# Optimization experiments

Hardware: AMD Instinct MI355X
Metric: run time of the kernel (lower is better)

## Reference

```python
import jax, jax.numpy as jnp
import numpy as np

K = 3
EPS = 1e-16

def setup_inputs() -> dict:
    key = jax.random.key(0)
    k1, k2, k3 = jax.random.split(key, 3)
    x = jax.random.normal(k1, (4096, 256), dtype=jnp.float32)
    pos_l = jax.random.normal(k2, (4096, 3), dtype=jnp.float32)
    pos_h = jax.random.normal(k3, (16384, 3), dtype=jnp.float32)
    return {"x": x, "pos_l": pos_l, "pos_h": pos_h}

def reference(x, pos_l, pos_h):
    # Squared pairwise distances [N_h, N_l] via expansion (GEMM-friendly)
    d2 = (jnp.sum(pos_h * pos_h, axis=1)[:, None]
          - 2.0 * pos_h @ pos_l.T
          + jnp.sum(pos_l * pos_l, axis=1)[None, :])
    # k nearest coarse neighbors per fine point
    _, idx = jax.lax.top_k(-d2, K)                      # idx: [N_h, K]
    # Recompute exact squared distances for selected neighbors (matches PyG knn_interpolate)
    diff = pos_h[:, None, :] - pos_l[idx]               # [N_h, K, D]
    d2_sel = jnp.sum(diff * diff, axis=-1)              # [N_h, K]
    w = 1.0 / jnp.clip(d2_sel, EPS)                     # inverse-distance weights
    feats = x[idx]                                      # [N_h, K, F]
    y = jnp.sum(feats * w[:, :, None], axis=1) / jnp.sum(w, axis=1, keepdims=True)
    return y
```

## Files before the change

kernel.cpp:

```cpp
#include <hip/hip_runtime.h>
#include <math.h>

#define NL    4096
#define NH    16384
#define NF4   64
#define BLK   1024
#define NW    16
#define FPB   64
#define HALF  2048
#define PERW  128

__device__ __forceinline__ void ins3(float d, int j,
    float& b0, float& b1, float& b2, int& i0, int& i1, int& i2)
{
  const bool p0 = d < b0;
  const bool p1 = d < b1;
  const bool p2 = d < b2;
  const int ni0 = p0 ? j : i0;
  const int ni1 = p0 ? i0 : (p1 ? j : i1);
  const int ni2 = p1 ? i1 : (p2 ? j : i2);
  const float nb0 = fminf(b0, d);
  const float nb1 = __builtin_amdgcn_fmed3f(d, b0, b1);
  const float nb2 = __builtin_amdgcn_fmed3f(d, b1, b2);
  b0 = nb0; b1 = nb1; b2 = nb2;
  i0 = ni0; i1 = ni1; i2 = ni2;
}

__device__ __forceinline__ void lexins3(float d, int j,
    float& b0, float& b1, float& b2, int& i0, int& i1, int& i2)
{
  bool s2 = (d < b2) || ((d == b2) && (j < i2));
  b2 = s2 ? d : b2;  i2 = s2 ? j : i2;
  bool s1 = (b2 < b1) || ((b2 == b1) && (i2 < i1));
  float tf = b1; int ti = i1;
  b1 = s1 ? b2 : b1;  i1 = s1 ? i2 : i1;
  b2 = s1 ? tf : b2;  i2 = s1 ? ti : i2;
  bool s0 = (b1 < b0) || ((b1 == b0) && (i1 < i0));
  tf = b0; ti = i0;
  b0 = s0 ? b1 : b0;  i0 = s0 ? i1 : i0;
  b1 = s0 ? tf : b1;  i1 = s0 ? ti : i1;
}

__global__ __launch_bounds__(BLK)
void knn_interp_kernel(const float* __restrict__ x,
                       const float* __restrict__ pos_l,
                       const float* __restrict__ pos_h,
                       float* __restrict__ out)
{
  __shared__ float4 pl4[HALF];
  __shared__ float  pd[NW * FPB * 3];
  __shared__ int    pj[NW * FPB * 3];
  __shared__ float  wn[FPB * 3];
  __shared__ int    sj[FPB * 3];

  const int tid  = threadIdx.x;
  const int lane = tid & 63;
  const int wv   = __builtin_amdgcn_readfirstlane(tid >> 6);
  const int fg   = blockIdx.x * FPB + lane;

  const float h0 = pos_h[fg * 3 + 0];
  const float h1 = pos_h[fg * 3 + 1];
  const float h2 = pos_h[fg * 3 + 2];
  const float hh = __fadd_rn(__fadd_rn(__fmul_rn(h0, h0), __fmul_rn(h1, h1)),
                             __fmul_rn(h2, h2));

  float a0 = INFINITY, a1 = INFINITY, a2 = INFINITY;  int ai0 = 0, ai1 = 0, ai2 = 0;
  float c0 = INFINITY, c1 = INFINITY, c2 = INFINITY;  int ci0 = 0, ci1 = 0, ci2 = 0;

  for (int half = 0; half < 2; ++half) {
    for (int p = tid; p < HALF; p += BLK) {
      const int g = half * HALF + p;
      const float l0 = pos_l[g * 3 + 0];
      const float l1 = pos_l[g * 3 + 1];
      const float l2 = pos_l[g * 3 + 2];
      const float ll = __fadd_rn(__fadd_rn(__fmul_rn(l0, l0), __fmul_rn(l1, l1)),
                                 __fmul_rn(l2, l2));
      pl4[p] = make_float4(l0, l1, l2, ll);
    }
    __syncthreads();

    const int base  = wv * PERW;
    const int jbase = half * HALF + base;

    #pragma unroll 8
    for (int t = 0; t < PERW; t += 2) {
      const float4 pa = pl4[base + t];
      const float4 pb = pl4[base + t + 1];
      const float dota = __fmaf_rn(h2, pa.z, __fmaf_rn(h1, pa.y, __fmul_rn(h0, pa.x)));
      const float da   = __fadd_rn(__fsub_rn(hh, __fmul_rn(2.0f, dota)), pa.w);
      const float dotb = __fmaf_rn(h2, pb.z, __fmaf_rn(h1, pb.y, __fmul_rn(h0, pb.x)));
      const float db   = __fadd_rn(__fsub_rn(hh, __fmul_rn(2.0f, dotb)), pb.w);
      ins3(da, jbase + t,     a0, a1, a2, ai0, ai1, ai2);
      ins3(db, jbase + t + 1, c0, c1, c2, ci0, ci1, ci2);
    }
    __syncthreads();
  }

  lexins3(c0, ci0, a0, a1, a2, ai0, ai1, ai2);
  lexins3(c1, ci1, a0, a1, a2, ai0, ai1, ai2);
  lexins3(c2, ci2, a0, a1, a2, ai0, ai1, ai2);

  {
    const int s = (wv * FPB + lane) * 3;
    pd[s + 0] = a0; pd[s + 1] = a1; pd[s + 2] = a2;
    pj[s + 0] = ai0; pj[s + 1] = ai1; pj[s + 2] = ai2;
  }
  __syncthreads();

  if (tid < FPB) {
    float b0 = INFINITY, b1 = INFINITY, b2 = INFINITY;
    int   i0 = 0x7fffffff, i1 = 0x7fffffff, i2 = 0x7fffffff;
    for (int w = 0; w < NW; ++w) {
      const int s = (w * FPB + tid) * 3;
      lexins3(pd[s + 0], pj[s + 0], b0, b1, b2, i0, i1, i2);
      lexins3(pd[s + 1], pj[s + 1], b0, b1, b2, i0, i1, i2);
      lexins3(pd[s + 2], pj[s + 2], b0, b1, b2, i0, i1, i2);
    }

    const int fm = blockIdx.x * FPB + tid;
    const float H0 = pos_h[fm * 3 + 0];
    const float H1 = pos_h[fm * 3 + 1];
    const float H2 = pos_h[fm * 3 + 2];

    float wk[3];
    int   jk[3] = { i0, i1, i2 };
    #pragma unroll
    for (int k = 0; k < 3; ++k) {
      const int j = jk[k];
      const float dx = __fsub_rn(H0, pos_l[j * 3 + 0]);
      const float dy = __fsub_rn(H1, pos_l[j * 3 + 1]);
      const float dz = __fsub_rn(H2, pos_l[j * 3 + 2]);
      float d2 = __fadd_rn(__fadd_rn(__fmul_rn(dx, dx), __fmul_rn(dy, dy)),
                           __fmul_rn(dz, dz));
      d2 = fmaxf(d2, 1e-16f);
      wk[k] = __frcp_rn(d2);
    }
    const float W  = __fadd_rn(__fadd_rn(wk[0], wk[1]), wk[2]);
    const float rW = __frcp_rn(W);
    #pragma unroll
    for (int k = 0; k < 3; ++k) {
      wn[tid * 3 + k] = wk[k] * rW;
      sj[tid * 3 + k] = jk[k];
    }
  }
  __syncthreads();

  const float4* __restrict__ x4   = (const float4*)x;
  float4* __restrict__       out4 = (float4*)out;
  #pragma unroll
  for (int i = 0; i < (FPB * NF4) / BLK; ++i) {
    const int task = tid + i * BLK;
    const int f    = task >> 6;
    const int cc   = task & 63;
    const int j0 = sj[f * 3 + 0], j1 = sj[f * 3 + 1], j2 = sj[f * 3 + 2];
    const float w0 = wn[f * 3 + 0], w1 = wn[f * 3 + 1], w2 = wn[f * 3 + 2];
    const float4 xa = x4[j0 * NF4 + cc];
    const float4 xb = x4[j1 * NF4 + cc];
    const float4 xc = x4[j2 * NF4 + cc];
    float4 r;
    r.x = xa.x * w0 + xb.x * w1 + xc.x * w2;
    r.y = xa.y * w0 + xb.y * w1 + xc.y * w2;
    r.z = xa.z * w0 + xb.z * w1 + xc.z * w2;
    r.w = xa.w * w0 + xb.w * w1 + xc.w * w2;
    out4[(blockIdx.x * FPB + f) * NF4 + cc] = r;
  }
}

extern "C" void kernel_launch(void* const* d_in, const int* in_sizes, int n_in,
                              void* d_out, int out_size, void* d_ws, size_t ws_size,
                              hipStream_t stream)
{
  const float* x     = (const float*)d_in[0];
  const float* pos_l = (const float*)d_in[1];
  const float* pos_h = (const float*)d_in[2];
  float* out = (float*)d_out;

  dim3 grid(NH / FPB);
  dim3 block(BLK);
  hipLaunchKernelGGL(knn_interp_kernel, grid, block, 0, stream, x, pos_l, pos_h, out);
}
```

Baseline: 113.0 us.

## Precompute packed coarse positions in prep kernel and read them via scalar loads

Adds a small prep kernel that packs pos_l into float4 (x,y,z,|l|^2) in workspace. The main kernel no longer stages candidates through LDS with two block-wide syncs. Each wave instead reads its own contiguous 256-candidate slice straight from global memory, using a wave-uniform base so the loads can become scalar/broadcast loads. This removes per-block staging and barriers, but adds a second kernel launch and depends on cache hits for the candidate stream.

```diff
diff --git a/kernel.cpp b/kernel.cpp
--- a/kernel.cpp
+++ b/kernel.cpp
@@ -7,8 +7,7 @@
 #define BLK   1024
 #define NW    16
 #define FPB   64
-#define HALF  2048
-#define PERW  128
+#define PERW  (NL / NW)
 
 __device__ __forceinline__ void ins3(float d, int j,
     float& b0, float& b1, float& b2, int& i0, int& i1, int& i2)
@@ -41,13 +40,25 @@
   b1 = s0 ? tf : b1;  i1 = s0 ? ti : i1;
 }
 
+__global__ __launch_bounds__(256)
+void prep_kernel(const float* __restrict__ pos_l, float4* __restrict__ cand)
+{
+  const int i = blockIdx.x * 256 + threadIdx.x;
+  const float l0 = pos_l[i * 3 + 0];
+  const float l1 = pos_l[i * 3 + 1];
+  const float l2 = pos_l[i * 3 + 2];
+  const float ll = __fadd_rn(__fadd_rn(__fmul_rn(l0, l0), __fmul_rn(l1, l1)),
+                             __fmul_rn(l2, l2));
+  cand[i] = make_float4(l0, l1, l2, ll);
+}
+
 __global__ __launch_bounds__(BLK)
 void knn_interp_kernel(const float* __restrict__ x,
                        const float* __restrict__ pos_l,
                        const float* __restrict__ pos_h,
+                       const float4* __restrict__ cand,
                        float* __restrict__ out)
 {
-  __shared__ float4 pl4[HALF];
   __shared__ float  pd[NW * FPB * 3];
   __shared__ int    pj[NW * FPB * 3];
   __shared__ float  wn[FPB * 3];
@@ -67,33 +78,18 @@
   float a0 = INFINITY, a1 = INFINITY, a2 = INFINITY;  int ai0 = 0, ai1 = 0, ai2 = 0;
   float c0 = INFINITY, c1 = INFINITY, c2 = INFINITY;  int ci0 = 0, ci1 = 0, ci2 = 0;
 
-  for (int half = 0; half < 2; ++half) {
-    for (int p = tid; p < HALF; p += BLK) {
-      const int g = half * HALF + p;
-      const float l0 = pos_l[g * 3 + 0];
-      const float l1 = pos_l[g * 3 + 1];
-      const float l2 = pos_l[g * 3 + 2];
-      const float ll = __fadd_rn(__fadd_rn(__fmul_rn(l0, l0), __fmul_rn(l1, l1)),
-                                 __fmul_rn(l2, l2));
-      pl4[p] = make_float4(l0, l1, l2, ll);
-    }
-    __syncthreads();
+  const int jbase = __builtin_amdgcn_readfirstlane(wv * PERW);
 
-    const int base  = wv * PERW;
-    const int jbase = half * HALF + base;
-
-    #pragma unroll 8
-    for (int t = 0; t < PERW; t += 2) {
-      const float4 pa = pl4[base + t];
-      const float4 pb = pl4[base + t + 1];
-      const float dota = __fmaf_rn(h2, pa.z, __fmaf_rn(h1, pa.y, __fmul_rn(h0, pa.x)));
-      const float da   = __fadd_rn(__fsub_rn(hh, __fmul_rn(2.0f, dota)), pa.w);
-      const float dotb = __fmaf_rn(h2, pb.z, __fmaf_rn(h1, pb.y, __fmul_rn(h0, pb.x)));
-      const float db   = __fadd_rn(__fsub_rn(hh, __fmul_rn(2.0f, dotb)), pb.w);
-      ins3(da, jbase + t,     a0, a1, a2, ai0, ai1, ai2);
-      ins3(db, jbase + t + 1, c0, c1, c2, ci0, ci1, ci2);
-    }
-    __syncthreads();
+  #pragma unroll 8
+  for (int t = 0; t < PERW; t += 2) {
+    const float4 pa = cand[jbase + t];
+    const float4 pb = cand[jbase + t + 1];
+    const float dota = __fmaf_rn(h2, pa.z, __fmaf_rn(h1, pa.y, __fmul_rn(h0, pa.x)));
+    const float da   = __fadd_rn(__fsub_rn(hh, __fmul_rn(2.0f, dota)), pa.w);
+    const float dotb = __fmaf_rn(h2, pb.z, __fmaf_rn(h1, pb.y, __fmul_rn(h0, pb.x)));
+    const float db   = __fadd_rn(__fsub_rn(hh, __fmul_rn(2.0f, dotb)), pb.w);
+    ins3(da, jbase + t,     a0, a1, a2, ai0, ai1, ai2);
+    ins3(db, jbase + t + 1, c0, c1, c2, ci0, ci1, ci2);
   }
 
   lexins3(c0, ci0, a0, a1, a2, ai0, ai1, ai2);
@@ -174,8 +170,10 @@
   const float* pos_l = (const float*)d_in[1];
   const float* pos_h = (const float*)d_in[2];
   float* out = (float*)d_out;
+  float4* cand = (float4*)d_ws;
 
-  dim3 grid(NH / FPB);
-  dim3 block(BLK);
-  hipLaunchKernelGGL(knn_interp_kernel, grid, block, 0, stream, x, pos_l, pos_h, out);
+  hipLaunchKernelGGL(prep_kernel, dim3(NL / 256), dim3(256), 0, stream,
+                     pos_l, cand);
+  hipLaunchKernelGGL(knn_interp_kernel, dim3(NH / FPB), dim3(BLK), 0, stream,
+                     x, pos_l, pos_h, cand, out);
 }
```

Result: slower. 120.5 us (+6.7%).
